# Kernel optimization log

Hardware: AMD Instinct MI355X
Metric: run time of the kernel (lower is better)

Reference implementation:

```python
import jax, jax.numpy as jnp
import numpy as np

H = 8          # num_heads
L = 256        # lifting_dim
DH = L // H    # head dim


def setup_inputs() -> dict:
    key = jax.random.key(0)
    ks = jax.random.split(key, 32)
    B, N, E = 4, 16384, 65536
    Dn, De, Dg = 128, 64, 32

    def lin_w(k, din, dout):
        return jax.random.normal(k, (din, dout), jnp.float32) * (din ** -0.5)

    inp = {
        "node_features": jax.random.normal(ks[0], (B, N, Dn), jnp.float32),
        "edge_features": jax.random.normal(ks[1], (B, E, De), jnp.float32),
        "energy": jax.random.normal(ks[2], (Dg,), jnp.float32),
        "W_node": lin_w(ks[3], Dn, L), "b_node": jnp.zeros((L,), jnp.float32),
        "W_edge": lin_w(ks[4], De, L), "b_edge": jnp.zeros((L,), jnp.float32),
        "W_graph": lin_w(ks[5], Dg, L), "b_graph": jnp.zeros((L,), jnp.float32),
        "Wq": lin_w(ks[6], L, L), "bq": jnp.zeros((L,), jnp.float32),
        # stacked per-hetero-type key/value projections: [3, L, L]
        "Wk": jnp.stack([lin_w(ks[7 + i], L, L) for i in range(3)]),
        "bk": jnp.zeros((3, L), jnp.float32),
        "Wv": jnp.stack([lin_w(ks[10 + i], L, L) for i in range(3)]),
        "bv": jnp.zeros((3, L), jnp.float32),
        "W_out": lin_w(ks[13], L, L), "b_out": jnp.zeros((L,), jnp.float32),
    }
    return inp


def _heads(x, B, T):
    # [B,T,L] -> [B,H,T,DH]
    return x.reshape(B, T, H, DH).transpose(0, 2, 1, 3)


def reference(node_features, edge_features, energy,
              W_node, b_node, W_edge, b_edge, W_graph, b_graph,
              Wq, bq, Wk, bk, Wv, bv, W_out, b_out):
    B, N, _ = node_features.shape
    lifted_nodes = node_features @ W_node + b_node            # [B,N,L]
    lifted_edges = edge_features @ W_edge + b_edge            # [B,E,L]
    lifted_graph = jnp.broadcast_to(energy, (B, 1, energy.shape[0])) @ W_graph + b_graph  # [B,1,L]

    hetero = [lifted_nodes, lifted_edges, lifted_graph]

    q = _heads(lifted_nodes @ Wq + bq, B, N)                  # [B,H,N,DH]
    q = jax.nn.softmax(q, axis=-1)

    out = None
    # NOTE: faithful to the original, `out` is overwritten each iteration,
    # so only the last hetero feature (graph) determines the output.
    for i in range(3):
        h = hetero[i]
        T = h.shape[1]
        k = jax.nn.softmax(_heads(h @ Wk[i] + bk[i], B, T), axis=-1)  # [B,H,T,DH]
        v = _heads(h @ Wv[i] + bv[i], B, T)                           # [B,H,T,DH]
        k_sum = k.sum(axis=-2, keepdims=True)                          # [B,H,1,DH]
        d_inv = 1.0 / jnp.clip((q * k_sum).sum(axis=-1, keepdims=True), 1e-8)  # [B,H,N,1]
        kv = jnp.einsum("bhtd,bhte->bhde", k, v)                       # [B,H,DH,DH]
        out = q + jnp.einsum("bhnd,bhde->bhne", q, kv) * d_inv         # [B,H,N,DH]

    out = out.transpose(0, 2, 1, 3).reshape(B, N, L)
    return out @ W_out + b_out
```

## Files before the change

### kernel.cpp

```cpp
#include <hip/hip_runtime.h>
#include <hip/hip_bf16.h>
#include <cstdint>
#include <cstddef>


typedef __attribute__((ext_vector_type(8))) short short8;
typedef __attribute__((ext_vector_type(4))) float floatx4;

using bf16 = __hip_bfloat16;

static constexpr int Mrows = 65536;
static constexpr int Lcols = 256;

static __device__ __forceinline__ short f2bs(float x) {
  bf16 h = __float2bfloat16(x);
  return *reinterpret_cast<short*>(&h);
}

__global__ void k_wnq(const float* __restrict__ Wn, const float* __restrict__ Wq,
                      short* __restrict__ wnq_t) {
  __shared__ float wqc[256];
  const int j = blockIdx.x, t = threadIdx.x;
  wqc[t] = Wq[t * 256 + j];
  wqc[t + 128] = Wq[(t + 128) * 256 + j];
  __syncthreads();
  const float* wr = Wn + t * 256;
  float acc = 0.f;
#pragma unroll 8
  for (int l = 0; l < 256; ++l) acc += wr[l] * wqc[l];
  wnq_t[j * 128 + t] = f2bs(acc);
}

__global__ void k_transpose_out(const float* __restrict__ src,
                                short* __restrict__ dst) {
  const int r = blockIdx.x, c = threadIdx.x;
  dst[c * 256 + r] = f2bs(src[r * 256 + c]);
}

__global__ void k_consts(const float* __restrict__ energy,
                         const float* __restrict__ W_graph,
                         const float* __restrict__ b_graph,
                         const float* __restrict__ Wk,
                         const float* __restrict__ bk,
                         const float* __restrict__ Wv,
                         const float* __restrict__ bv,
                         const float* __restrict__ b_node,
                         const float* __restrict__ Wq,
                         const float* __restrict__ bq,
                         float* __restrict__ klbuf,
                         float* __restrict__ vvec,
                         float* __restrict__ bnq) {
  __shared__ float ev[32];
  __shared__ float r0[256], r1[256], r2[256];
  const int j = blockIdx.x, d = threadIdx.x;
  if (d < 32) ev[d] = energy[d];
  __syncthreads();

  float lgd = b_graph[d];
#pragma unroll
  for (int e = 0; e < 32; ++e) lgd += ev[e] * W_graph[e * 256 + d];

  r0[d] = lgd * Wk[2 * 65536 + d * 256 + j];
  r1[d] = lgd * Wv[2 * 65536 + d * 256 + j];
  r2[d] = b_node[d] * Wq[d * 256 + j];
  __syncthreads();
  for (int s = 128; s > 0; s >>= 1) {
    if (d < s) { r0[d] += r0[d + s]; r1[d] += r1[d + s]; r2[d] += r2[d + s]; }
    __syncthreads();
  }
  if (d == 0) {
    klbuf[j] = r0[0] + bk[512 + j];
    vvec[j]  = r1[0] + bv[512 + j];
    bnq[j]   = r2[0] + bq[j];
  }
}

__global__ void k_softmax_k(const float* __restrict__ klbuf,
                            float* __restrict__ kvec) {
  __shared__ float kl[256];
  const int j = threadIdx.x;
  kl[j] = klbuf[j];
  __syncthreads();
  const int h0 = j & ~31;
  float mx = -1e30f;
  for (int t = 0; t < 32; ++t) mx = fmaxf(mx, kl[h0 + t]);
  float s = 0.f;
  for (int t = 0; t < 32; ++t) s += __expf(kl[h0 + t] - mx);
  kvec[j] = __expf(kl[j] - mx) / s;
}

__global__ __launch_bounds__(256, 3)
void k_fused(const float* __restrict__ nf,
             const short* __restrict__ wnq,
             const short* __restrict__ wto,
             const float* __restrict__ bnq,
             const float* __restrict__ kvec,
             const float* __restrict__ vvec,
             const float* __restrict__ b_out,
             float* __restrict__ out) {
  constexpr int AS_STR = 136;
  constexpr int WB_STR = 40;
  constexpr int PS_STR = 264;
  constexpr int WOFF1  = 64 * AS_STR;
  constexpr int WOFF2  = 64 * PS_STR;
  __shared__ short smem[WOFF2 + 256 * WB_STR];

  const int t = threadIdx.x;
  const int lane = t & 63;
  const int l15 = lane & 15;
  const int lhi = lane >> 4;
  const int cw = (t >> 6) * 64;
  const int rowBase = blockIdx.x * 64;

  {
    const int row = t >> 2;
    const int c0 = (t & 3) << 5;
    const float* src = nf + (size_t)(rowBase + row) * 128 + c0;
    short tmp[32];
#pragma unroll
    for (int i = 0; i < 8; ++i) {
      float4 f = *(const float4*)(src + i * 4);
      tmp[i * 4 + 0] = f2bs(f.x); tmp[i * 4 + 1] = f2bs(f.y);
      tmp[i * 4 + 2] = f2bs(f.z); tmp[i * 4 + 3] = f2bs(f.w);
    }
#pragma unroll
    for (int i = 0; i < 4; ++i)
      *(short8*)(&smem[row * AS_STR + c0 + i * 8]) = *(short8*)(&tmp[i * 8]);
  }

  floatx4 acc[4][4];
#pragma unroll
  for (int m = 0; m < 4; ++m)
#pragma unroll
    for (int n = 0; n < 4; ++n) acc[m][n] = (floatx4){0.f, 0.f, 0.f, 0.f};

  for (int kc = 0; kc < 4; ++kc) {
    {
      const short* src = wnq + t * 128 + kc * 32;
      short8 w0 = *(const short8*)(src);
      short8 w1 = *(const short8*)(src + 8);
      short8 w2 = *(const short8*)(src + 16);
      short8 w3 = *(const short8*)(src + 24);
      short* dst = &smem[WOFF1 + t * WB_STR];
      *(short8*)(dst) = w0;      *(short8*)(dst + 8) = w1;
      *(short8*)(dst + 16) = w2; *(short8*)(dst + 24) = w3;
    }
    __syncthreads();
    short8 af[4], bfv[4];
#pragma unroll
    for (int m = 0; m < 4; ++m)
      af[m] = *(const short8*)(&smem[(m * 16 + l15) * AS_STR + kc * 32 + lhi * 8]);
#pragma unroll
    for (int n = 0; n < 4; ++n)
      bfv[n] = *(const short8*)(&smem[WOFF1 + (cw + n * 16 + l15) * WB_STR + lhi * 8]);
#pragma unroll
    for (int m = 0; m < 4; ++m)
#pragma unroll
      for (int n = 0; n < 4; ++n)
        acc[m][n] = __builtin_amdgcn_mfma_f32_16x16x32_bf16(af[m], bfv[n],
                                                            acc[m][n], 0, 0, 0);
    __syncthreads();
  }

#pragma unroll
  for (int tt = 0; tt < 2; ++tt) {
    const int col0 = cw + tt * 32 + l15;
    const int col1 = col0 + 16;
    const float b0 = bnq[col0], b1 = bnq[col1];
    const float k0v = kvec[col0], k1v = kvec[col1];
    const float v0v = vvec[col0], v1v = vvec[col1];
#pragma unroll
    for (int m = 0; m < 4; ++m) {
      const int row0 = m * 16 + lhi * 4;
#pragma unroll
      for (int r = 0; r < 4; ++r) {
        float e0 = __expf(acc[m][2 * tt][r] + b0);
        float e1 = __expf(acc[m][2 * tt + 1][r] + b1);
        float s = e0 + e1;
        float du = e0 * k0v + e1 * k1v;
#pragma unroll
        for (int msk = 1; msk <= 8; msk <<= 1) {
          s += __shfl_xor(s, msk);
          du += __shfl_xor(du, msk);
        }
        float inv = 1.0f / s;
        float d = du * inv;
        float ratio = d / fmaxf(d, 1e-8f);
        smem[(row0 + r) * PS_STR + col0] = f2bs(e0 * inv + v0v * ratio);
        smem[(row0 + r) * PS_STR + col1] = f2bs(e1 * inv + v1v * ratio);
      }
    }
  }
#pragma unroll
  for (int m = 0; m < 4; ++m)
#pragma unroll
    for (int n = 0; n < 4; ++n) acc[m][n] = (floatx4){0.f, 0.f, 0.f, 0.f};
  __syncthreads();

  for (int kc = 0; kc < 8; ++kc) {
    {
      const short* src = wto + t * 256 + kc * 32;
      short8 w0 = *(const short8*)(src);
      short8 w1 = *(const short8*)(src + 8);
      short8 w2 = *(const short8*)(src + 16);
      short8 w3 = *(const short8*)(src + 24);
      short* dst = &smem[WOFF2 + t * WB_STR];
      *(short8*)(dst) = w0;      *(short8*)(dst + 8) = w1;
      *(short8*)(dst + 16) = w2; *(short8*)(dst + 24) = w3;
    }
    __syncthreads();
    short8 af[4], bfv[4];
#pragma unroll
    for (int m = 0; m < 4; ++m)
      af[m] = *(const short8*)(&smem[(m * 16 + l15) * PS_STR + kc * 32 + lhi * 8]);
#pragma unroll
    for (int n = 0; n < 4; ++n)
      bfv[n] = *(const short8*)(&smem[WOFF2 + (cw + n * 16 + l15) * WB_STR + lhi * 8]);
#pragma unroll
    for (int m = 0; m < 4; ++m)
#pragma unroll
      for (int n = 0; n < 4; ++n)
        acc[m][n] = __builtin_amdgcn_mfma_f32_16x16x32_bf16(af[m], bfv[n],
                                                            acc[m][n], 0, 0, 0);
    __syncthreads();
  }

#pragma unroll
  for (int n = 0; n < 4; ++n) {
    const int col = cw + n * 16 + l15;
    const float bb = b_out[col];
#pragma unroll
    for (int m = 0; m < 4; ++m) {
      const int row0 = rowBase + m * 16 + lhi * 4;
#pragma unroll
      for (int r = 0; r < 4; ++r)
        out[(size_t)(row0 + r) * Lcols + col] = acc[m][n][r] + bb;
    }
  }
}

extern "C" void kernel_launch(void* const* d_in, const int* in_sizes, int n_in,
                              void* d_out, int out_size, void* d_ws, size_t ws_size,
                              hipStream_t stream) {
  const float* node_features = (const float*)d_in[0];
  const float* energy  = (const float*)d_in[2];
  const float* W_node  = (const float*)d_in[3];
  const float* b_node  = (const float*)d_in[4];
  const float* W_graph = (const float*)d_in[7];
  const float* b_graph = (const float*)d_in[8];
  const float* Wq      = (const float*)d_in[9];
  const float* bq      = (const float*)d_in[10];
  const float* Wk      = (const float*)d_in[11];
  const float* bk      = (const float*)d_in[12];
  const float* Wv      = (const float*)d_in[13];
  const float* bv      = (const float*)d_in[14];
  const float* W_out   = (const float*)d_in[15];
  const float* b_out   = (const float*)d_in[16];

  char* ws = (char*)d_ws;
  short* wnq_t = (short*)(ws);
  short* wto_t = (short*)(ws + 65536);
  float* klbuf = (float*)(ws + 196608);
  float* kvec  = (float*)(ws + 197632);
  float* vvec  = (float*)(ws + 198656);
  float* bnq   = (float*)(ws + 199680);

  k_wnq<<<dim3(256), dim3(128), 0, stream>>>(W_node, Wq, wnq_t);
  k_transpose_out<<<dim3(256), dim3(256), 0, stream>>>(W_out, wto_t);
  k_consts<<<dim3(256), dim3(256), 0, stream>>>(
      energy, W_graph, b_graph, Wk, bk, Wv, bv, b_node, Wq, bq,
      klbuf, vvec, bnq);
  k_softmax_k<<<dim3(1), dim3(256), 0, stream>>>(klbuf, kvec);

  k_fused<<<dim3(Mrows / 64), dim3(256), 0, stream>>>(
      node_features, wnq_t, wto_t, bnq, kvec, vvec, b_out, (float*)d_out);
}
```

Before: 215.1 us.

## Merge setup kernels and load GEMM weight fragments directly from global memory

The three weight/constant preprocessing kernels become one multi-role launch, and the single-block key softmax is folded into the fused kernel, where each block recomputes it. The fused kernel no longer stages weight tiles through shared memory with barriers each k-step. It reads B fragments straight from global memory (cached in L2/L1) instead. The smaller LDS footprint allows a launch-bounds occupancy of 4. This removes launch overhead and per-step syncs, at the cost of uncoalesced-ish global fragment loads and redundant softmax work per block.

```diff
diff --git a/kernel.cpp b/kernel.cpp
--- a/kernel.cpp
+++ b/kernel.cpp
@@ -17,93 +17,82 @@
   return *reinterpret_cast<short*>(&h);
 }
 
-__global__ void k_wnq(const float* __restrict__ Wn, const float* __restrict__ Wq,
-                      short* __restrict__ wnq_t) {
-  __shared__ float wqc[256];
-  const int j = blockIdx.x, t = threadIdx.x;
-  wqc[t] = Wq[t * 256 + j];
-  wqc[t + 128] = Wq[(t + 128) * 256 + j];
-  __syncthreads();
-  const float* wr = Wn + t * 256;
-  float acc = 0.f;
+__global__ void k_setup(const float* __restrict__ W_node,
+                        const float* __restrict__ Wq,
+                        const float* __restrict__ W_out,
+                        const float* __restrict__ energy,
+                        const float* __restrict__ W_graph,
+                        const float* __restrict__ b_graph,
+                        const float* __restrict__ Wk,
+                        const float* __restrict__ bk,
+                        const float* __restrict__ Wv,
+                        const float* __restrict__ bv,
+                        const float* __restrict__ b_node,
+                        const float* __restrict__ bq,
+                        short* __restrict__ wnq_t,
+                        short* __restrict__ wto_t,
+                        float* __restrict__ klbuf,
+                        float* __restrict__ vvec,
+                        float* __restrict__ bnq) {
+  const int b = blockIdx.x;
+  const int t = threadIdx.x;
+
+  if (b < 256) {
+    __shared__ float wqc[256];
+    const int j = b;
+    wqc[t] = Wq[t * 256 + j];
+    __syncthreads();
+    if (t < 128) {
+      const float* wr = W_node + t * 256;
+      float acc = 0.f;
 #pragma unroll 8
-  for (int l = 0; l < 256; ++l) acc += wr[l] * wqc[l];
-  wnq_t[j * 128 + t] = f2bs(acc);
-}
-
-__global__ void k_transpose_out(const float* __restrict__ src,
-                                short* __restrict__ dst) {
-  const int r = blockIdx.x, c = threadIdx.x;
-  dst[c * 256 + r] = f2bs(src[r * 256 + c]);
-}
-
-__global__ void k_consts(const float* __restrict__ energy,
-                         const float* __restrict__ W_graph,
-                         const float* __restrict__ b_graph,
-                         const float* __restrict__ Wk,
-                         const float* __restrict__ bk,
-                         const float* __restrict__ Wv,
-                         const float* __restrict__ bv,
-                         const float* __restrict__ b_node,
-                         const float* __restrict__ Wq,
-                         const float* __restrict__ bq,
-                         float* __restrict__ klbuf,
-                         float* __restrict__ vvec,
-                         float* __restrict__ bnq) {
-  __shared__ float ev[32];
-  __shared__ float r0[256], r1[256], r2[256];
-  const int j = blockIdx.x, d = threadIdx.x;
-  if (d < 32) ev[d] = energy[d];
-  __syncthreads();
-
-  float lgd = b_graph[d];
-#pragma unroll
-  for (int e = 0; e < 32; ++e) lgd += ev[e] * W_graph[e * 256 + d];
-
-  r0[d] = lgd * Wk[2 * 65536 + d * 256 + j];
-  r1[d] = lgd * Wv[2 * 65536 + d * 256 + j];
-  r2[d] = b_node[d] * Wq[d * 256 + j];
-  __syncthreads();
-  for (int s = 128; s > 0; s >>= 1) {
-    if (d < s) { r0[d] += r0[d + s]; r1[d] += r1[d + s]; r2[d] += r2[d + s]; }
+      for (int l = 0; l < 256; ++l) acc += wr[l] * wqc[l];
+      wnq_t[j * 128 + t] = f2bs(acc);
+    }
+  } else if (b < 512) {
+    const int r = b - 256;
+    wto_t[t * 256 + r] = f2bs(W_out[r * 256 + t]);
+  } else {
+    __shared__ float ev[32];
+    __shared__ float r0[256], r1[256], r2[256];
+    const int j = b - 512, d = t;
+    if (d < 32) ev[d] = energy[d];
     __syncthreads();
-  }
-  if (d == 0) {
-    klbuf[j] = r0[0] + bk[512 + j];
-    vvec[j]  = r1[0] + bv[512 + j];
-    bnq[j]   = r2[0] + bq[j];
-  }
-}
-
-__global__ void k_softmax_k(const float* __restrict__ klbuf,
-                            float* __restrict__ kvec) {
-  __shared__ float kl[256];
-  const int j = threadIdx.x;
-  kl[j] = klbuf[j];
-  __syncthreads();
-  const int h0 = j & ~31;
-  float mx = -1e30f;
-  for (int t = 0; t < 32; ++t) mx = fmaxf(mx, kl[h0 + t]);
-  float s = 0.f;
-  for (int t = 0; t < 32; ++t) s += __expf(kl[h0 + t] - mx);
-  kvec[j] = __expf(kl[j] - mx) / s;
-}
-
-__global__ __launch_bounds__(256, 3)
+
+    float lgd = b_graph[d];
+#pragma unroll
+    for (int e = 0; e < 32; ++e) lgd += ev[e] * W_graph[e * 256 + d];
+
+    r0[d] = lgd * Wk[2 * 65536 + d * 256 + j];
+    r1[d] = lgd * Wv[2 * 65536 + d * 256 + j];
+    r2[d] = b_node[d] * Wq[d * 256 + j];
+    __syncthreads();
+    for (int s = 128; s > 0; s >>= 1) {
+      if (d < s) { r0[d] += r0[d + s]; r1[d] += r1[d + s]; r2[d] += r2[d + s]; }
+      __syncthreads();
+    }
+    if (d == 0) {
+      klbuf[j] = r0[0] + bk[512 + j];
+      vvec[j]  = r1[0] + bv[512 + j];
+      bnq[j]   = r2[0] + bq[j];
+    }
+  }
+}
+
+__global__ __launch_bounds__(256, 4)
 void k_fused(const float* __restrict__ nf,
              const short* __restrict__ wnq,
              const short* __restrict__ wto,
+             const float* __restrict__ klbuf,
              const float* __restrict__ bnq,
-             const float* __restrict__ kvec,
              const float* __restrict__ vvec,
              const float* __restrict__ b_out,
              float* __restrict__ out) {
   constexpr int AS_STR = 136;
-  constexpr int WB_STR = 40;
   constexpr int PS_STR = 264;
-  constexpr int WOFF1  = 64 * AS_STR;
-  constexpr int WOFF2  = 64 * PS_STR;
-  __shared__ short smem[WOFF2 + 256 * WB_STR];
+  __shared__ short smem[64 * PS_STR];
+  __shared__ float kl[256];
+  __shared__ float kv[256];
 
   const int t = threadIdx.x;
   const int lane = t & 63;
@@ -112,6 +101,8 @@
   const int cw = (t >> 6) * 64;
   const int rowBase = blockIdx.x * 64;
 
+  kl[t] = klbuf[t];
+
   {
     const int row = t >> 2;
     const int c0 = (t & 3) << 5;
@@ -127,6 +118,18 @@
     for (int i = 0; i < 4; ++i)
       *(short8*)(&smem[row * AS_STR + c0 + i * 8]) = *(short8*)(&tmp[i * 8]);
   }
+  __syncthreads();
+
+  {
+    const int h0 = t & ~31;
+    float mx = -1e30f;
+#pragma unroll 8
+    for (int i = 0; i < 32; ++i) mx = fmaxf(mx, kl[h0 + i]);
+    float s = 0.f;
+#pragma unroll 8
+    for (int i = 0; i < 32; ++i) s += __expf(kl[h0 + i] - mx);
+    kv[t] = __expf(kl[t] - mx) / s;
+  }
 
   floatx4 acc[4][4];
 #pragma unroll
@@ -134,40 +137,33 @@
 #pragma unroll
     for (int n = 0; n < 4; ++n) acc[m][n] = (floatx4){0.f, 0.f, 0.f, 0.f};
 
-  for (int kc = 0; kc < 4; ++kc) {
-    {
-      const short* src = wnq + t * 128 + kc * 32;
-      short8 w0 = *(const short8*)(src);
-      short8 w1 = *(const short8*)(src + 8);
-      short8 w2 = *(const short8*)(src + 16);
-      short8 w3 = *(const short8*)(src + 24);
-      short* dst = &smem[WOFF1 + t * WB_STR];
-      *(short8*)(dst) = w0;      *(short8*)(dst + 8) = w1;
-      *(short8*)(dst + 16) = w2; *(short8*)(dst + 24) = w3;
-    }
-    __syncthreads();
-    short8 af[4], bfv[4];
-#pragma unroll
-    for (int m = 0; m < 4; ++m)
-      af[m] = *(const short8*)(&smem[(m * 16 + l15) * AS_STR + kc * 32 + lhi * 8]);
-#pragma unroll
-    for (int n = 0; n < 4; ++n)
-      bfv[n] = *(const short8*)(&smem[WOFF1 + (cw + n * 16 + l15) * WB_STR + lhi * 8]);
-#pragma unroll
-    for (int m = 0; m < 4; ++m)
+  {
+    const short* wb = wnq + (cw + l15) * 128 + lhi * 8;
+#pragma unroll
+    for (int kc = 0; kc < 4; ++kc) {
+      short8 af[4], bfv[4];
 #pragma unroll
       for (int n = 0; n < 4; ++n)
-        acc[m][n] = __builtin_amdgcn_mfma_f32_16x16x32_bf16(af[m], bfv[n],
-                                                            acc[m][n], 0, 0, 0);
-    __syncthreads();
-  }
+        bfv[n] = *(const short8*)(wb + n * 16 * 128 + kc * 32);
+#pragma unroll
+      for (int m = 0; m < 4; ++m)
+        af[m] = *(const short8*)(&smem[(m * 16 + l15) * AS_STR + kc * 32 + lhi * 8]);
+#pragma unroll
+      for (int m = 0; m < 4; ++m)
+#pragma unroll
+        for (int n = 0; n < 4; ++n)
+          acc[m][n] = __builtin_amdgcn_mfma_f32_16x16x32_bf16(af[m], bfv[n],
+                                                              acc[m][n], 0, 0, 0);
+    }
+  }
+  __syncthreads();
 
 #pragma unroll
   for (int tt = 0; tt < 2; ++tt) {
     const int col0 = cw + tt * 32 + l15;
     const int col1 = col0 + 16;
     const float b0 = bnq[col0], b1 = bnq[col1];
-    const float k0v = kvec[col0], k1v = kvec[col1];
+    const float k0v = kv[col0], k1v = kv[col1];
     const float v0v = vvec[col0], v1v = vvec[col1];
 #pragma unroll
     for (int m = 0; m < 4; ++m) {
@@ -197,32 +193,24 @@
     for (int n = 0; n < 4; ++n) acc[m][n] = (floatx4){0.f, 0.f, 0.f, 0.f};
   __syncthreads();
 
-  for (int kc = 0; kc < 8; ++kc) {
-    {
-      const short* src = wto + t * 256 + kc * 32;
-      short8 w0 = *(const short8*)(src);
-      short8 w1 = *(const short8*)(src + 8);
-      short8 w2 = *(const short8*)(src + 16);
-      short8 w3 = *(const short8*)(src + 24);
-      short* dst = &smem[WOFF2 + t * WB_STR];
-      *(short8*)(dst) = w0;      *(short8*)(dst + 8) = w1;
-      *(short8*)(dst + 16) = w2; *(short8*)(dst + 24) = w3;
-    }
-    __syncthreads();
-    short8 af[4], bfv[4];
-#pragma unroll
-    for (int m = 0; m < 4; ++m)
-      af[m] = *(const short8*)(&smem[(m * 16 + l15) * PS_STR + kc * 32 + lhi * 8]);
-#pragma unroll
-    for (int n = 0; n < 4; ++n)
-      bfv[n] = *(const short8*)(&smem[WOFF2 + (cw + n * 16 + l15) * WB_STR + lhi * 8]);
-#pragma unroll
-    for (int m = 0; m < 4; ++m)
+  {
+    const short* wb = wto + (cw + l15) * 256 + lhi * 8;
+#pragma unroll
+    for (int kc = 0; kc < 8; ++kc) {
+      short8 af[4], bfv[4];
 #pragma unroll
       for (int n = 0; n < 4; ++n)
-        acc[m][n] = __builtin_amdgcn_mfma_f32_16x16x32_bf16(af[m], bfv[n],
-                                                            acc[m][n], 0, 0, 0);
-    __syncthreads();
+        bfv[n] = *(const short8*)(wb + n * 16 * 256 + kc * 32);
+#pragma unroll
+      for (int m = 0; m < 4; ++m)
+        af[m] = *(const short8*)(&smem[(m * 16 + l15) * PS_STR + kc * 32 + lhi * 8]);
+#pragma unroll
+      for (int m = 0; m < 4; ++m)
+#pragma unroll
+        for (int n = 0; n < 4; ++n)
+          acc[m][n] = __builtin_amdgcn_mfma_f32_16x16x32_bf16(af[m], bfv[n],
+                                                              acc[m][n], 0, 0, 0);
+    }
   }
 
 #pragma unroll
@@ -261,17 +249,13 @@
   short* wnq_t = (short*)(ws);
   short* wto_t = (short*)(ws + 65536);
   float* klbuf = (float*)(ws + 196608);
-  float* kvec  = (float*)(ws + 197632);
-  float* vvec  = (float*)(ws + 198656);
-  float* bnq   = (float*)(ws + 199680);
-
-  k_wnq<<<dim3(256), dim3(128), 0, stream>>>(W_node, Wq, wnq_t);
-  k_transpose_out<<<dim3(256), dim3(256), 0, stream>>>(W_out, wto_t);
-  k_consts<<<dim3(256), dim3(256), 0, stream>>>(
-      energy, W_graph, b_graph, Wk, bk, Wv, bv, b_node, Wq, bq,
-      klbuf, vvec, bnq);
-  k_softmax_k<<<dim3(1), dim3(256), 0, stream>>>(klbuf, kvec);
+  float* vvec  = (float*)(ws + 197632);
+  float* bnq   = (float*)(ws + 198656);
+
+  k_setup<<<dim3(768), dim3(256), 0, stream>>>(
+      W_node, Wq, W_out, energy, W_graph, b_graph, Wk, bk, Wv, bv,
+      b_node, bq, wnq_t, wto_t, klbuf, vvec, bnq);
 
   k_fused<<<dim3(Mrows / 64), dim3(256), 0, stream>>>(
-      node_features, wnq_t, wto_t, bnq, kvec, vvec, b_out, (float*)d_out);
-}
+      node_features, wnq_t, wto_t, klbuf, bnq, vvec, b_out, (float*)d_out);
+}
```

Result: faster. 196.8 us (-8.5%).
